# Kernel optimization log

Hardware: AMD Instinct MI355X
Metric: run time of the kernel (lower is better)

Reference implementation:

```python
import jax, jax.numpy as jnp
import numpy as np

B, N, D, H, P = 16, 1024, 768, 12, 16
HD = D // H
FF = 4 * D
SCALE = HD ** -0.5


def _layer_norm(x, g, b, eps=1e-5):
    mu = jnp.mean(x, axis=-1, keepdims=True)
    var = jnp.var(x, axis=-1, keepdims=True)
    return (x - mu) * jax.lax.rsqrt(var + eps) * g + b


def setup_inputs() -> dict:
    key = jax.random.key(0)
    ks = jax.random.split(key, 8)
    s = 0.02
    return {
        "x": jax.random.normal(ks[0], (B, N, D), jnp.float32),
        "prompt": jax.random.normal(ks[1], (B, 2, P, H, HD), jnp.float32),
        "qkv_w": jax.random.normal(ks[2], (3 * D, D), jnp.float32) * s,
        "qkv_b": jnp.zeros((3 * D,), jnp.float32),
        "out_w": jax.random.normal(ks[3], (D, D), jnp.float32) * s,
        "out_b": jnp.zeros((D,), jnp.float32),
        "ln1_g": jnp.ones((D,), jnp.float32),
        "ln1_b": jnp.zeros((D,), jnp.float32),
        "ln2_g": jnp.ones((D,), jnp.float32),
        "ln2_b": jnp.zeros((D,), jnp.float32),
        "fc1_w": jax.random.normal(ks[4], (FF, D), jnp.float32) * s,
        "fc1_b": jnp.zeros((FF,), jnp.float32),
        "fc2_w": jax.random.normal(ks[5], (D, FF), jnp.float32) * s,
        "fc2_b": jnp.zeros((D,), jnp.float32),
    }


def reference(x, prompt, qkv_w, qkv_b, out_w, out_b, ln1_g, ln1_b,
              ln2_g, ln2_b, fc1_w, fc1_b, fc2_w, fc2_b):
    # --- attention branch ---
    h = _layer_norm(x, ln1_g, ln1_b)                       # [B,N,D]
    qkv = h @ qkv_w.T + qkv_b                              # [B,N,3D]
    qkv = qkv.reshape(B, N, 3, H, HD).transpose(2, 0, 3, 1, 4)  # [3,B,H,N,hd]
    q, k, v = qkv[0], qkv[1], qkv[2]
    # prompt [B,2,P,H,hd] -> [2,B,H,P,hd]
    pr = jnp.transpose(prompt, (1, 0, 3, 2, 4))
    k = jnp.concatenate([pr[0], k], axis=2)                # [B,H,P+N,hd]
    v = jnp.concatenate([pr[1], v], axis=2)
    attn = jnp.einsum("bhqd,bhkd->bhqk", q, k) * SCALE     # [B,H,N,P+N]
    attn = jax.nn.softmax(attn, axis=-1)
    o = jnp.einsum("bhqk,bhkd->bhqd", attn, v)             # [B,H,N,hd]
    o = o.transpose(0, 2, 1, 3).reshape(B, N, D)
    o = o @ out_w.T + out_b
    x = x + o
    # --- MLP branch (CLIP: c_fc -> QuickGELU -> c_proj) ---
    h2 = _layer_norm(x, ln2_g, ln2_b)
    m = h2 @ fc1_w.T + fc1_b
    m = m * jax.nn.sigmoid(1.702 * m)                      # QuickGELU
    m = m @ fc2_w.T + fc2_b
    return x + m
```

## Files before the change

### kernel.cpp

```cpp
#include <hip/hip_runtime.h>
#include <hip/hip_bf16.h>

typedef __bf16 bf16;
typedef __attribute__((ext_vector_type(8))) __bf16 bf16x8;
typedef __attribute__((ext_vector_type(4))) __bf16 bf16x4;
typedef __attribute__((ext_vector_type(4))) float f32x4;

#define GLOBAL_AS __attribute__((address_space(1)))
#define LDS_AS __attribute__((address_space(3)))

constexpr int B_  = 16;
constexpr int N_  = 1024;
constexpr int D_  = 768;
constexpr int H_  = 12;
constexpr int P_  = 16;
constexpr int FF_ = 3072;
constexpr int BN_ = B_ * N_;
constexpr int LP_ = 1088;
constexpr float EXPC_ = 0.18033688f;

__global__ __launch_bounds__(256) void cvt_kernel(
    const float* __restrict__ s0, const float* __restrict__ s1,
    const float* __restrict__ s2, const float* __restrict__ s3,
    bf16* __restrict__ d0, bf16* __restrict__ d1,
    bf16* __restrict__ d2, bf16* __restrict__ d3)
{
    int i = (blockIdx.x * 256 + threadIdx.x) * 4;
    const float* s; bf16* d; int off;
    if (i < 1769472)      { s = s0; d = d0; off = i; }
    else if (i < 2359296) { s = s1; d = d1; off = i - 1769472; }
    else if (i < 4718592) { s = s2; d = d2; off = i - 2359296; }
    else                  { s = s3; d = d3; off = i - 4718592; }
    float4 f = *(const float4*)(s + off);
    bf16x4 o;
    o[0] = (bf16)f.x; o[1] = (bf16)f.y; o[2] = (bf16)f.z; o[3] = (bf16)f.w;
    *(bf16x4*)(d + off) = o;
}

__global__ __launch_bounds__(256) void prep_kernel(
    const float* __restrict__ prompt, bf16* __restrict__ Kall,
    bf16* __restrict__ VTall)
{
    int hb = blockIdx.x;
    int b = hb / 12, h = hb % 12;
    int t = threadIdx.x;
    size_t kbase = (size_t)hb * LP_ * 64;
    size_t vbase = (size_t)hb * 64 * LP_;

    {
        int p = t >> 4, d0 = (t & 15) * 4;
        const float* src = prompt + (((size_t)(b * 2 + 0) * P_ + p) * H_ + h) * 64 + d0;
        float4 f = *(const float4*)src;
        bf16x4 o4;
        o4[0] = (bf16)f.x; o4[1] = (bf16)f.y; o4[2] = (bf16)f.z; o4[3] = (bf16)f.w;
        *(bf16x4*)(Kall + kbase + (size_t)p * 64 + d0) = o4;
    }
    {
        int d = t >> 2, p0 = (t & 3) * 4;
        bf16x4 o4;
#pragma unroll
        for (int j = 0; j < 4; j++)
            o4[j] = (bf16)prompt[(((size_t)(b * 2 + 1) * P_ + p0 + j) * H_ + h) * 64 + d];
        *(bf16x4*)(VTall + vbase + (size_t)d * LP_ + p0) = o4;
    }
    {
        bf16* kp = Kall + kbase + 1040 * 64 + (size_t)t * 12;
#pragma unroll
        for (int i = 0; i < 12; i++) kp[i] = (bf16)0.f;
        int d = t >> 2, j0 = (t & 3) * 12;
        bf16* vp = VTall + vbase + (size_t)d * LP_ + 1040 + j0;
#pragma unroll
        for (int i = 0; i < 12; i++) vp[i] = (bf16)0.f;
    }
}

template <typename T>
__global__ __launch_bounds__(256) void ln_kernel(
    const T* __restrict__ x, const float* __restrict__ g,
    const float* __restrict__ bta, bf16* __restrict__ out)
{
    int row = blockIdx.x;
    const T* xr = x + (size_t)row * D_;
    int t = threadIdx.x;
    float v[3];
    float s = 0.f, ss = 0.f;
#pragma unroll
    for (int i = 0; i < 3; i++) {
        v[i] = (float)xr[t + i * 256];
        s += v[i];
        ss += v[i] * v[i];
    }
#pragma unroll
    for (int o = 32; o > 0; o >>= 1) {
        s  += __shfl_down(s, o);
        ss += __shfl_down(ss, o);
    }
    __shared__ float red_s[4], red_ss[4];
    int w = t >> 6, lane = t & 63;
    if (lane == 0) { red_s[w] = s; red_ss[w] = ss; }
    __syncthreads();
    s  = red_s[0] + red_s[1] + red_s[2] + red_s[3];
    ss = red_ss[0] + red_ss[1] + red_ss[2] + red_ss[3];
    float mu = s * (1.f / 768.f);
    float var = ss * (1.f / 768.f) - mu * mu;
    float rstd = rsqrtf(var + 1e-5f);
#pragma unroll
    for (int i = 0; i < 3; i++) {
        int c = t + i * 256;
        out[(size_t)row * D_ + c] = (bf16)((v[i] - mu) * rstd * g[c] + bta[c]);
    }
}

template <int EPI>
__global__ __launch_bounds__(256, 2) void gemm_bt(
    const bf16* __restrict__ A, const bf16* __restrict__ Bt,
    const float* __restrict__ bias,
    const float* __restrict__ resF, const bf16* __restrict__ resB,
    float* __restrict__ outF, bf16* __restrict__ outB,
    bf16* __restrict__ Qall, bf16* __restrict__ Kall, bf16* __restrict__ VTall,
    int M, int N, int K)
{
    __shared__ bf16 As[128 * 64];
    __shared__ bf16 Bs[128 * 64];

    const int tid = threadIdx.x;
    const int w = tid >> 6, lane = tid & 63;
    const int wr = w >> 1, wc = w & 1;
    const int lrow = lane & 15, khalf = lane >> 4;
    const int rowBase = blockIdx.y * 128;
    const int colBase = blockIdx.x * 128;

    f32x4 acc[4][4];
#pragma unroll
    for (int mi = 0; mi < 4; mi++)
#pragma unroll
        for (int ni = 0; ni < 4; ni++)
            acc[mi][ni] = (f32x4){0.f, 0.f, 0.f, 0.f};

    for (int k0 = 0; k0 < K; k0 += 64) {
#pragma unroll
        for (int i = 0; i < 4; i++) {
            int idx = i * 256 + w * 64 + lane;
            int r = idx >> 3, c = idx & 7;
            int cs = c ^ (r & 7);
            __builtin_amdgcn_global_load_lds(
                (const GLOBAL_AS void*)(A + (size_t)(rowBase + r) * K + k0 + cs * 8),
                (LDS_AS void*)(As + (size_t)idx * 8), 16, 0, 0);
        }
#pragma unroll
        for (int i = 0; i < 4; i++) {
            int idx = i * 256 + w * 64 + lane;
            int r = idx >> 3, c = idx & 7;
            int cs = c ^ (r & 7);
            __builtin_amdgcn_global_load_lds(
                (const GLOBAL_AS void*)(Bt + (size_t)(colBase + r) * K + k0 + cs * 8),
                (LDS_AS void*)(Bs + (size_t)idx * 8), 16, 0, 0);
        }
        __syncthreads();

#pragma unroll
        for (int ks = 0; ks < 2; ks++) {
            bf16x8 af[4], bfr[4];
#pragma unroll
            for (int mi = 0; mi < 4; mi++) {
                int rr = wr * 64 + mi * 16 + lrow;
                int ch = (ks * 4 + khalf) ^ (rr & 7);
                af[mi] = *(const bf16x8*)(As + (size_t)rr * 64 + ch * 8);
            }
#pragma unroll
            for (int ni = 0; ni < 4; ni++) {
                int rr = wc * 64 + ni * 16 + lrow;
                int ch = (ks * 4 + khalf) ^ (rr & 7);
                bfr[ni] = *(const bf16x8*)(Bs + (size_t)rr * 64 + ch * 8);
            }
#pragma unroll
            for (int mi = 0; mi < 4; mi++)
#pragma unroll
                for (int ni = 0; ni < 4; ni++)
                    acc[mi][ni] = __builtin_amdgcn_mfma_f32_16x16x32_bf16(
                        af[mi], bfr[ni], acc[mi][ni], 0, 0, 0);
        }
        __syncthreads();
    }

#pragma unroll
    for (int mi = 0; mi < 4; mi++) {
#pragma unroll
        for (int ni = 0; ni < 4; ni++) {
            int col = colBase + wc * 64 + ni * 16 + lrow;
            int row0 = rowBase + wr * 64 + mi * 16 + khalf * 4;
            float bv = bias[col];
            if constexpr (EPI == 3) {
                int sect = (col >= 1536) ? 2 : (col >= 768 ? 1 : 0);
                int hh = (col >> 6) - sect * 12;
                int dd = col & 63;
                int bb = row0 >> 10, n0 = row0 & 1023;
                size_t bh = (size_t)bb * 12 + hh;
                if (sect == 0) {
                    bf16* qp = Qall + (bh * 1024 + n0) * 64 + dd;
#pragma unroll
                    for (int r = 0; r < 4; r++)
                        qp[(size_t)r * 64] = (bf16)(acc[mi][ni][r] + bv);
                } else if (sect == 1) {
                    bf16* kp = Kall + bh * (LP_ * 64) + (size_t)(16 + n0) * 64 + dd;
#pragma unroll
                    for (int r = 0; r < 4; r++)
                        kp[(size_t)r * 64] = (bf16)(acc[mi][ni][r] + bv);
                } else {
                    bf16x4 pv;
#pragma unroll
                    for (int r = 0; r < 4; r++)
                        pv[r] = (bf16)(acc[mi][ni][r] + bv);
                    *(bf16x4*)(VTall + bh * (64 * LP_) + (size_t)dd * LP_ + 16 + n0) = pv;
                }
            } else {
#pragma unroll
                for (int r = 0; r < 4; r++) {
                    size_t idx = (size_t)(row0 + r) * N + col;
                    float v = acc[mi][ni][r] + bv;
                    if constexpr (EPI == 1) {
                        outF[idx] = v + (float)resB[idx];
                    } else if constexpr (EPI == 2) {
                        outB[idx] = (bf16)(v / (1.f + __expf(-1.702f * v)));
                    } else {
                        outB[idx] = (bf16)(v + resF[idx]);
                    }
                }
            }
        }
    }
}

__global__ __launch_bounds__(256, 2) void attn_kernel(
    const bf16* __restrict__ Qall, const bf16* __restrict__ Kall,
    const bf16* __restrict__ VTall, bf16* __restrict__ o)
{
    __shared__ bf16 Qs[128 * 64];
    __shared__ bf16 Ks[64 * 64];
    __shared__ bf16 Vt[64 * 64];
    __shared__ bf16 Ps[4 * 32 * 72];

    const int lid = blockIdx.x;
    const int xcd = lid & 7, slot = lid >> 3;
    const int hb = xcd * 24 + (slot >> 3);
    const int qt = slot & 7;
    const int h = hb % 12, b = hb / 12;

    const int tid = threadIdx.x;
    const int w = tid >> 6, lane = tid & 63;
    const int lrow = lane & 15, q4 = lane >> 4;

    const bf16* qb = Qall + ((size_t)hb * 1024 + qt * 128) * 64;
#pragma unroll
    for (int i = 0; i < 4; i++) {
        int idx = i * 256 + w * 64 + lane;
        int r = idx >> 3, c = idx & 7, cs = c ^ (r & 7);
        __builtin_amdgcn_global_load_lds(
            (const GLOBAL_AS void*)(qb + (size_t)r * 64 + cs * 8),
            (LDS_AS void*)(Qs + (size_t)idx * 8), 16, 0, 0);
    }

    f32x4 acc_o[2][4];
    float lp[2][4];
#pragma unroll
    for (int mi = 0; mi < 2; mi++) {
#pragma unroll
        for (int ni = 0; ni < 4; ni++) acc_o[mi][ni] = (f32x4){0.f, 0.f, 0.f, 0.f};
#pragma unroll
        for (int r = 0; r < 4; r++) lp[mi][r] = 0.f;
    }

    const bf16* kb = Kall + (size_t)hb * LP_ * 64;
    const bf16* vb = VTall + (size_t)hb * 64 * LP_;
    bf16* pw = Ps + w * (32 * 72);

    for (int kt = 0; kt < 17; kt++) {
        __syncthreads();
#pragma unroll
        for (int i = 0; i < 2; i++) {
            int idx = w * 128 + i * 64 + lane;
            int r = idx >> 3, c = idx & 7, cs = c ^ (r & 7);
            __builtin_amdgcn_global_load_lds(
                (const GLOBAL_AS void*)(kb + (size_t)kt * 4096 + (size_t)r * 64 + cs * 8),
                (LDS_AS void*)(Ks + (size_t)idx * 8), 16, 0, 0);
        }
#pragma unroll
        for (int i = 0; i < 2; i++) {
            int idx = w * 128 + i * 64 + lane;
            int r = idx >> 3, c = idx & 7, cs = c ^ (r & 7);
            __builtin_amdgcn_global_load_lds(
                (const GLOBAL_AS void*)(vb + (size_t)r * LP_ + kt * 64 + cs * 8),
                (LDS_AS void*)(Vt + (size_t)idx * 8), 16, 0, 0);
        }
        __syncthreads();

        const int ntile = (kt == 16) ? 1 : 4;
        f32x4 accs[2][4];
#pragma unroll
        for (int mi = 0; mi < 2; mi++)
#pragma unroll
            for (int ni = 0; ni < 4; ni++) accs[mi][ni] = (f32x4){0.f, 0.f, 0.f, 0.f};

#pragma unroll
        for (int ks = 0; ks < 2; ks++) {
            bf16x8 qf[2];
#pragma unroll
            for (int mi = 0; mi < 2; mi++) {
                int rr = w * 32 + mi * 16 + lrow;
                int ch = ks * 4 + q4;
                qf[mi] = *(const bf16x8*)(Qs + (size_t)rr * 64 + ((ch ^ (rr & 7)) * 8));
            }
#pragma unroll
            for (int ni = 0; ni < 4; ni++) {
                if (ni >= ntile) continue;
                int rr = ni * 16 + lrow;
                int ch = ks * 4 + q4;
                bf16x8 kf = *(const bf16x8*)(Ks + (size_t)rr * 64 + ((ch ^ (rr & 7)) * 8));
                accs[0][ni] = __builtin_amdgcn_mfma_f32_16x16x32_bf16(qf[0], kf, accs[0][ni], 0, 0, 0);
                accs[1][ni] = __builtin_amdgcn_mfma_f32_16x16x32_bf16(qf[1], kf, accs[1][ni], 0, 0, 0);
            }
        }

#pragma unroll
        for (int mi = 0; mi < 2; mi++) {
#pragma unroll
            for (int r = 0; r < 4; r++) {
                int prow = mi * 16 + q4 * 4 + r;
                float psum = 0.f;
#pragma unroll
                for (int ni = 0; ni < 4; ni++) {
                    float p = (kt == 16 && ni > 0) ? 0.f
                              : exp2f(accs[mi][ni][r] * EXPC_);
                    pw[(size_t)prow * 72 + ni * 16 + lrow] = (bf16)p;
                    psum += p;
                }
                lp[mi][r] += psum;
            }
        }

#pragma unroll
        for (int ks = 0; ks < 2; ks++) {
            bf16x8 pf[2];
#pragma unroll
            for (int mi = 0; mi < 2; mi++)
                pf[mi] = *(const bf16x8*)(pw + (size_t)(mi * 16 + lrow) * 72 + ks * 32 + q4 * 8);
#pragma unroll
            for (int ni = 0; ni < 4; ni++) {
                bf16x8 vf = *(const bf16x8*)(Vt + (size_t)(ni * 16 + lrow) * 64 +
                                             (((ks * 4 + q4) ^ ((ni * 16 + lrow) & 7)) * 8));
                acc_o[0][ni] = __builtin_amdgcn_mfma_f32_16x16x32_bf16(pf[0], vf, acc_o[0][ni], 0, 0, 0);
                acc_o[1][ni] = __builtin_amdgcn_mfma_f32_16x16x32_bf16(pf[1], vf, acc_o[1][ni], 0, 0, 0);
            }
        }
    }

    float linv[2][4];
#pragma unroll
    for (int mi = 0; mi < 2; mi++)
#pragma unroll
        for (int r = 0; r < 4; r++) {
            float ls = lp[mi][r];
#pragma unroll
            for (int sft = 1; sft < 16; sft <<= 1) ls += __shfl_xor(ls, sft);
            linv[mi][r] = 1.f / ls;
        }

    bf16* ob = o + (size_t)(b * N_ + qt * 128 + w * 32) * 768 + h * 64;
#pragma unroll
    for (int mi = 0; mi < 2; mi++)
#pragma unroll
        for (int ni = 0; ni < 4; ni++)
#pragma unroll
            for (int r = 0; r < 4; r++) {
                int row = mi * 16 + q4 * 4 + r;
                ob[(size_t)row * 768 + ni * 16 + lrow] =
                    (bf16)(acc_o[mi][ni][r] * linv[mi][r]);
            }
}

extern "C" void kernel_launch(void* const* d_in, const int* in_sizes, int n_in,
                              void* d_out, int out_size, void* d_ws, size_t ws_size,
                              hipStream_t stream)
{
    const float* x      = (const float*)d_in[0];
    const float* prompt = (const float*)d_in[1];
    const float* qkv_w  = (const float*)d_in[2];
    const float* qkv_b  = (const float*)d_in[3];
    const float* out_w  = (const float*)d_in[4];
    const float* out_b  = (const float*)d_in[5];
    const float* ln1_g  = (const float*)d_in[6];
    const float* ln1_b  = (const float*)d_in[7];
    const float* ln2_g  = (const float*)d_in[8];
    const float* ln2_b  = (const float*)d_in[9];
    const float* fc1_w  = (const float*)d_in[10];
    const float* fc1_b  = (const float*)d_in[11];
    const float* fc2_w  = (const float*)d_in[12];
    const float* fc2_b  = (const float*)d_in[13];
    float* out = (float*)d_out;

    bf16* qkvw_b = (bf16*)d_ws;
    bf16* outw_b = qkvw_b + 1769472;
    bf16* fc1w_b = outw_b + 589824;
    bf16* fc2w_b = fc1w_b + 2359296;
    bf16* h_b    = fc2w_b + 2359296;
    bf16* o_b    = h_b    + 12582912;
    bf16* Qall   = o_b    + 12582912;
    bf16* Kall   = Qall   + 12582912;
    bf16* VTall  = Kall   + 13369344;
    bf16* mid    = o_b;
    bf16* x1b    = VTall + 13369344;

    cvt_kernel<<<6912, 256, 0, stream>>>(qkv_w, out_w, fc1_w, fc2_w,
                                         qkvw_b, outw_b, fc1w_b, fc2w_b);
    prep_kernel<<<192, 256, 0, stream>>>(prompt, Kall, VTall);
    ln_kernel<float><<<BN_, 256, 0, stream>>>(x, ln1_g, ln1_b, h_b);
    gemm_bt<3><<<dim3(18, 128), 256, 0, stream>>>(h_b, qkvw_b, qkv_b, nullptr, nullptr,
                                                  nullptr, nullptr, Qall, Kall, VTall,
                                                  BN_, 2304, 768);
    attn_kernel<<<1536, 256, 0, stream>>>(Qall, Kall, VTall, o_b);
    gemm_bt<4><<<dim3(6, 128), 256, 0, stream>>>(o_b, outw_b, out_b, x, nullptr,
                                                 nullptr, x1b, nullptr, nullptr, nullptr,
                                                 BN_, 768, 768);
    ln_kernel<bf16><<<BN_, 256, 0, stream>>>(x1b, ln2_g, ln2_b, h_b);
    gemm_bt<2><<<dim3(24, 128), 256, 0, stream>>>(h_b, fc1w_b, fc1_b, nullptr, nullptr,
                                                  nullptr, mid, nullptr, nullptr, nullptr,
                                                  BN_, FF_, 768);
    gemm_bt<1><<<dim3(6, 128), 256, 0, stream>>>(mid, fc2w_b, fc2_b, nullptr, x1b,
                                                 out, nullptr, nullptr, nullptr, nullptr,
                                                 BN_, 768, FF_);
}
```

Before: 571.8 us.

## Keep P in registers via transposed S=K·Q^T and double-buffer K/V tiles

The attention kernel now computes scores as K·Q^T so each lane's accumulator holds a column of probabilities that feeds the PV MFMA (16x16x16) directly from registers. This removes the per-warp LDS P buffer. Q is kept in registers instead of LDS, and the softmax scale is folded into Q in the QKV epilogue. K/V tiles are double-buffered with register prefetch of the next tile and a single barrier per iteration. Less LDS allows raising occupancy to 3 blocks per CU, at the cost of register pressure and a smaller-K MFMA for PV. The last tile's padded keys are still exponentiated and fed into PV, relying on the zero-padded V columns for correctness.

```diff
diff --git a/kernel.cpp b/kernel.cpp
--- a/kernel.cpp
+++ b/kernel.cpp
@@ -4,6 +4,7 @@
 typedef __bf16 bf16;
 typedef __attribute__((ext_vector_type(8))) __bf16 bf16x8;
 typedef __attribute__((ext_vector_type(4))) __bf16 bf16x4;
+typedef __attribute__((ext_vector_type(4))) short s16x4;
 typedef __attribute__((ext_vector_type(4))) float f32x4;
 
 #define GLOBAL_AS __attribute__((address_space(1)))
@@ -200,7 +201,7 @@
                     bf16* qp = Qall + (bh * 1024 + n0) * 64 + dd;
 #pragma unroll
                     for (int r = 0; r < 4; r++)
-                        qp[(size_t)r * 64] = (bf16)(acc[mi][ni][r] + bv);
+                        qp[(size_t)r * 64] = (bf16)((acc[mi][ni][r] + bv) * EXPC_);
                 } else if (sect == 1) {
                     bf16* kp = Kall + bh * (LP_ * 64) + (size_t)(16 + n0) * 64 + dd;
 #pragma unroll
@@ -231,14 +232,12 @@
     }
 }
 
-__global__ __launch_bounds__(256, 2) void attn_kernel(
+__global__ __launch_bounds__(256, 3) void attn_kernel(
     const bf16* __restrict__ Qall, const bf16* __restrict__ Kall,
     const bf16* __restrict__ VTall, bf16* __restrict__ o)
 {
-    __shared__ bf16 Qs[128 * 64];
-    __shared__ bf16 Ks[64 * 64];
-    __shared__ bf16 Vt[64 * 64];
-    __shared__ bf16 Ps[4 * 32 * 72];
+    __shared__ bf16 Ks[2][64 * 72];
+    __shared__ bf16 Vt[2][64 * 72];
 
     const int lid = blockIdx.x;
     const int xcd = lid & 7, slot = lid >> 3;
@@ -250,132 +249,118 @@
     const int w = tid >> 6, lane = tid & 63;
     const int lrow = lane & 15, q4 = lane >> 4;
 
-    const bf16* qb = Qall + ((size_t)hb * 1024 + qt * 128) * 64;
-#pragma unroll
-    for (int i = 0; i < 4; i++) {
-        int idx = i * 256 + w * 64 + lane;
-        int r = idx >> 3, c = idx & 7, cs = c ^ (r & 7);
-        __builtin_amdgcn_global_load_lds(
-            (const GLOBAL_AS void*)(qb + (size_t)r * 64 + cs * 8),
-            (LDS_AS void*)(Qs + (size_t)idx * 8), 16, 0, 0);
-    }
-
-    f32x4 acc_o[2][4];
-    float lp[2][4];
+    bf16x8 qf[2][2];
+    {
+        const bf16* qb = Qall + ((size_t)hb * 1024 + qt * 128 + w * 32 + lrow) * 64 + q4 * 8;
+        qf[0][0] = *(const bf16x8*)(qb);
+        qf[0][1] = *(const bf16x8*)(qb + 32);
+        qf[1][0] = *(const bf16x8*)(qb + 16 * 64);
+        qf[1][1] = *(const bf16x8*)(qb + 16 * 64 + 32);
+    }
+
+    f32x4 acc_o[4][2];
+#pragma unroll
+    for (int dj = 0; dj < 4; dj++)
+#pragma unroll
+        for (int mi = 0; mi < 2; mi++)
+            acc_o[dj][mi] = (f32x4){0.f, 0.f, 0.f, 0.f};
+    float lp[2] = {0.f, 0.f};
+
+    const bf16* kg = Kall + (size_t)hb * LP_ * 64;
+    const bf16* vg = VTall + (size_t)hb * 64 * LP_;
+    const int r_ = tid >> 2;
+    const int c_ = (tid & 3) * 16;
+
+    bf16x8 k0 = *(const bf16x8*)(kg + (size_t)r_ * 64 + c_);
+    bf16x8 k1 = *(const bf16x8*)(kg + (size_t)r_ * 64 + c_ + 8);
+    bf16x8 v0 = *(const bf16x8*)(vg + (size_t)r_ * LP_ + c_);
+    bf16x8 v1 = *(const bf16x8*)(vg + (size_t)r_ * LP_ + c_ + 8);
+
+    for (int kt = 0; kt < 17; kt++) {
+        bf16* ksb = &Ks[kt & 1][0];
+        bf16* vtb = &Vt[kt & 1][0];
+        *(bf16x8*)(ksb + r_ * 72 + c_)     = k0;
+        *(bf16x8*)(ksb + r_ * 72 + c_ + 8) = k1;
+        *(bf16x8*)(vtb + r_ * 72 + c_)     = v0;
+        *(bf16x8*)(vtb + r_ * 72 + c_ + 8) = v1;
+        __syncthreads();
+
+        int nkt = (kt < 16) ? kt + 1 : 16;
+        k0 = *(const bf16x8*)(kg + (size_t)nkt * 4096 + (size_t)r_ * 64 + c_);
+        k1 = *(const bf16x8*)(kg + (size_t)nkt * 4096 + (size_t)r_ * 64 + c_ + 8);
+        v0 = *(const bf16x8*)(vg + (size_t)r_ * LP_ + nkt * 64 + c_);
+        v1 = *(const bf16x8*)(vg + (size_t)r_ * LP_ + nkt * 64 + c_ + 8);
+
+        f32x4 st[4][2];
+#pragma unroll
+        for (int kb = 0; kb < 4; kb++)
+#pragma unroll
+            for (int mi = 0; mi < 2; mi++)
+                st[kb][mi] = (f32x4){0.f, 0.f, 0.f, 0.f};
+#pragma unroll
+        for (int kb = 0; kb < 4; kb++) {
+#pragma unroll
+            for (int ks = 0; ks < 2; ks++) {
+                bf16x8 kf = *(const bf16x8*)(ksb + (size_t)(kb * 16 + lrow) * 72 +
+                                             ks * 32 + q4 * 8);
+                st[kb][0] = __builtin_amdgcn_mfma_f32_16x16x32_bf16(kf, qf[0][ks], st[kb][0], 0, 0, 0);
+                st[kb][1] = __builtin_amdgcn_mfma_f32_16x16x32_bf16(kf, qf[1][ks], st[kb][1], 0, 0, 0);
+            }
+        }
+
+        s16x4 pfrag[4][2];
+#pragma unroll
+        for (int kb = 0; kb < 4; kb++) {
+#pragma unroll
+            for (int mi = 0; mi < 2; mi++) {
+                float e0 = __builtin_amdgcn_exp2f(st[kb][mi][0]);
+                float e1 = __builtin_amdgcn_exp2f(st[kb][mi][1]);
+                float e2 = __builtin_amdgcn_exp2f(st[kb][mi][2]);
+                float e3 = __builtin_amdgcn_exp2f(st[kb][mi][3]);
+                if (kt < 16 || kb == 0)
+                    lp[mi] += (e0 + e1) + (e2 + e3);
+                bf16x4 pb;
+                pb[0] = (bf16)e0; pb[1] = (bf16)e1; pb[2] = (bf16)e2; pb[3] = (bf16)e3;
+                pfrag[kb][mi] = __builtin_bit_cast(s16x4, pb);
+            }
+        }
+
+#pragma unroll
+        for (int dj = 0; dj < 4; dj++) {
+#pragma unroll
+            for (int kb = 0; kb < 4; kb++) {
+                bf16x4 vf = *(const bf16x4*)(vtb + (size_t)(dj * 16 + lrow) * 72 +
+                                             kb * 16 + q4 * 4);
+                s16x4 vfs = __builtin_bit_cast(s16x4, vf);
+                acc_o[dj][0] = __builtin_amdgcn_mfma_f32_16x16x16bf16_1k(
+                    vfs, pfrag[kb][0], acc_o[dj][0], 0, 0, 0);
+                acc_o[dj][1] = __builtin_amdgcn_mfma_f32_16x16x16bf16_1k(
+                    vfs, pfrag[kb][1], acc_o[dj][1], 0, 0, 0);
+            }
+        }
+    }
+
+    float linv[2];
 #pragma unroll
     for (int mi = 0; mi < 2; mi++) {
-#pragma unroll
-        for (int ni = 0; ni < 4; ni++) acc_o[mi][ni] = (f32x4){0.f, 0.f, 0.f, 0.f};
-#pragma unroll
-        for (int r = 0; r < 4; r++) lp[mi][r] = 0.f;
-    }
-
-    const bf16* kb = Kall + (size_t)hb * LP_ * 64;
-    const bf16* vb = VTall + (size_t)hb * 64 * LP_;
-    bf16* pw = Ps + w * (32 * 72);
-
-    for (int kt = 0; kt < 17; kt++) {
-        __syncthreads();
-#pragma unroll
-        for (int i = 0; i < 2; i++) {
-            int idx = w * 128 + i * 64 + lane;
-            int r = idx >> 3, c = idx & 7, cs = c ^ (r & 7);
-            __builtin_amdgcn_global_load_lds(
-                (const GLOBAL_AS void*)(kb + (size_t)kt * 4096 + (size_t)r * 64 + cs * 8),
-                (LDS_AS void*)(Ks + (size_t)idx * 8), 16, 0, 0);
-        }
-#pragma unroll
-        for (int i = 0; i < 2; i++) {
-            int idx = w * 128 + i * 64 + lane;
-            int r = idx >> 3, c = idx & 7, cs = c ^ (r & 7);
-            __builtin_amdgcn_global_load_lds(
-                (const GLOBAL_AS void*)(vb + (size_t)r * LP_ + kt * 64 + cs * 8),
-                (LDS_AS void*)(Vt + (size_t)idx * 8), 16, 0, 0);
-        }
-        __syncthreads();
-
-        const int ntile = (kt == 16) ? 1 : 4;
-        f32x4 accs[2][4];
-#pragma unroll
-        for (int mi = 0; mi < 2; mi++)
-#pragma unroll
-            for (int ni = 0; ni < 4; ni++) accs[mi][ni] = (f32x4){0.f, 0.f, 0.f, 0.f};
-
-#pragma unroll
-        for (int ks = 0; ks < 2; ks++) {
-            bf16x8 qf[2];
-#pragma unroll
-            for (int mi = 0; mi < 2; mi++) {
-                int rr = w * 32 + mi * 16 + lrow;
-                int ch = ks * 4 + q4;
-                qf[mi] = *(const bf16x8*)(Qs + (size_t)rr * 64 + ((ch ^ (rr & 7)) * 8));
-            }
-#pragma unroll
-            for (int ni = 0; ni < 4; ni++) {
-                if (ni >= ntile) continue;
-                int rr = ni * 16 + lrow;
-                int ch = ks * 4 + q4;
-                bf16x8 kf = *(const bf16x8*)(Ks + (size_t)rr * 64 + ((ch ^ (rr & 7)) * 8));
-                accs[0][ni] = __builtin_amdgcn_mfma_f32_16x16x32_bf16(qf[0], kf, accs[0][ni], 0, 0, 0);
-                accs[1][ni] = __builtin_amdgcn_mfma_f32_16x16x32_bf16(qf[1], kf, accs[1][ni], 0, 0, 0);
-            }
-        }
-
-#pragma unroll
-        for (int mi = 0; mi < 2; mi++) {
-#pragma unroll
-            for (int r = 0; r < 4; r++) {
-                int prow = mi * 16 + q4 * 4 + r;
-                float psum = 0.f;
-#pragma unroll
-                for (int ni = 0; ni < 4; ni++) {
-                    float p = (kt == 16 && ni > 0) ? 0.f
-                              : exp2f(accs[mi][ni][r] * EXPC_);
-                    pw[(size_t)prow * 72 + ni * 16 + lrow] = (bf16)p;
-                    psum += p;
-                }
-                lp[mi][r] += psum;
-            }
-        }
-
-#pragma unroll
-        for (int ks = 0; ks < 2; ks++) {
-            bf16x8 pf[2];
-#pragma unroll
-            for (int mi = 0; mi < 2; mi++)
-                pf[mi] = *(const bf16x8*)(pw + (size_t)(mi * 16 + lrow) * 72 + ks * 32 + q4 * 8);
-#pragma unroll
-            for (int ni = 0; ni < 4; ni++) {
-                bf16x8 vf = *(const bf16x8*)(Vt + (size_t)(ni * 16 + lrow) * 64 +
-                                             (((ks * 4 + q4) ^ ((ni * 16 + lrow) & 7)) * 8));
-                acc_o[0][ni] = __builtin_amdgcn_mfma_f32_16x16x32_bf16(pf[0], vf, acc_o[0][ni], 0, 0, 0);
-                acc_o[1][ni] = __builtin_amdgcn_mfma_f32_16x16x32_bf16(pf[1], vf, acc_o[1][ni], 0, 0, 0);
-            }
-        }
-    }
-
-    float linv[2][4];
-#pragma unroll
-    for (int mi = 0; mi < 2; mi++)
-#pragma unroll
-        for (int r = 0; r < 4; r++) {
-            float ls = lp[mi][r];
-#pragma unroll
-            for (int sft = 1; sft < 16; sft <<= 1) ls += __shfl_xor(ls, sft);
-            linv[mi][r] = 1.f / ls;
-        }
+        float ls = lp[mi];
+        ls += __shfl_xor(ls, 16);
+        ls += __shfl_xor(ls, 32);
+        linv[mi] = 1.f / ls;
+    }
 
     bf16* ob = o + (size_t)(b * N_ + qt * 128 + w * 32) * 768 + h * 64;
 #pragma unroll
-    for (int mi = 0; mi < 2; mi++)
-#pragma unroll
-        for (int ni = 0; ni < 4; ni++)
-#pragma unroll
-            for (int r = 0; r < 4; r++) {
-                int row = mi * 16 + q4 * 4 + r;
-                ob[(size_t)row * 768 + ni * 16 + lrow] =
-                    (bf16)(acc_o[mi][ni][r] * linv[mi][r]);
-            }
+    for (int mi = 0; mi < 2; mi++) {
+#pragma unroll
+        for (int dj = 0; dj < 4; dj++) {
+            bf16x4 ov;
+#pragma unroll
+            for (int r = 0; r < 4; r++)
+                ov[r] = (bf16)(acc_o[dj][mi][r] * linv[mi]);
+            *(bf16x4*)(ob + (size_t)(mi * 16 + lrow) * 768 + dj * 16 + q4 * 4) = ov;
+        }
+    }
 }
 
 extern "C" void kernel_launch(void* const* d_in, const int* in_sizes, int n_in,
```

Measured after the change: 548.5 us. 1.04x faster.
